# Kernel tuning notes

Hardware: AMD Instinct MI355X
Metric: run time of the kernel (lower is better)

The kernel has to match this reference:

```python
import jax, jax.numpy as jnp
import numpy as np

N_NODES = 50000
N_EDGES = 600000
EMB_DIM = 128
NUM_LAYERS = 5
NUM_ELEM = 118
NUM_CHIR = 4
NUM_BOND_TYPE = 4
NUM_BOND_DIR = 3
BN_EPS = 1e-5


def _xavier(key, shape):
    fan_in, fan_out = shape[0], shape[1]
    limit = np.sqrt(6.0 / (fan_in + fan_out))
    return jax.random.uniform(key, shape, jnp.float32, -limit, limit)


def setup_inputs() -> dict:
    key = jax.random.key(0)
    ks = jax.random.split(key, 12)
    x = jax.random.randint(ks[0], (N_NODES, 2), 0, 4, dtype=jnp.int64)
    edge_index = jax.random.randint(ks[1], (2, N_EDGES), 0, N_NODES, dtype=jnp.int64)
    edge_attr = jax.random.randint(ks[2], (N_EDGES, 2), 0, 3, dtype=jnp.int64)
    elem_emb = _xavier(ks[3], (NUM_ELEM, EMB_DIM))
    chir_emb = _xavier(ks[4], (NUM_CHIR, EMB_DIM))
    bond_type_emb = _xavier(ks[5], (NUM_BOND_TYPE, EMB_DIM))
    bond_dir_emb = _xavier(ks[6], (NUM_BOND_DIR, EMB_DIM))
    # shared GINEConv MLP: Linear(D, 2D) -> ReLU -> Linear(2D, D)
    W1 = _xavier(ks[7], (EMB_DIM, 2 * EMB_DIM))
    b1 = jnp.zeros((2 * EMB_DIM,), jnp.float32)
    W2 = _xavier(ks[8], (2 * EMB_DIM, EMB_DIM))
    b2 = jnp.zeros((EMB_DIM,), jnp.float32)
    # per-layer BatchNorm affine params
    bn_gamma = jnp.ones((NUM_LAYERS, EMB_DIM), jnp.float32)
    bn_beta = jnp.zeros((NUM_LAYERS, EMB_DIM), jnp.float32)
    return {
        "x": x, "edge_index": edge_index, "edge_attr": edge_attr,
        "elem_emb": elem_emb, "chir_emb": chir_emb,
        "bond_type_emb": bond_type_emb, "bond_dir_emb": bond_dir_emb,
        "W1": W1, "b1": b1, "W2": W2, "b2": b2,
        "bn_gamma": bn_gamma, "bn_beta": bn_beta,
    }


def reference(x, edge_index, edge_attr, elem_emb, chir_emb,
              bond_type_emb, bond_dir_emb, W1, b1, W2, b2,
              bn_gamma, bn_beta):
    # input embeddings
    h = elem_emb[x[:, 0]] + chir_emb[x[:, 1]]                    # [N, D]
    e = bond_type_emb[edge_attr[:, 0]] + bond_dir_emb[edge_attr[:, 1]]  # [E, D]
    src, dst = edge_index[0], edge_index[1]
    n = h.shape[0]
    num_layers = bn_gamma.shape[0]
    for layer in range(num_layers):  # conv weights shared across layers
        # GINEConv: msg = relu(x_j + edge_attr), scatter-add, eps=0
        msg = jax.nn.relu(h[src] + e)                            # [E, D]
        agg = jax.ops.segment_sum(msg, dst, num_segments=n)      # [N, D]
        z = h + agg
        out = jax.nn.relu(z @ W1 + b1) @ W2 + b2                 # [N, D]
        # BatchNorm1d (training mode: batch stats, biased variance)
        mean = out.mean(axis=0)
        var = out.var(axis=0)
        out = (out - mean) * jax.lax.rsqrt(var + BN_EPS) * bn_gamma[layer] + bn_beta[layer]
        h = out if layer == num_layers - 1 else jax.nn.relu(out)
    return h
```

## Files before the change

### kernel.cpp

```cpp
#include <hip/hip_runtime.h>

typedef _Float16 f16;
typedef _Float16 f16x8 __attribute__((ext_vector_type(8)));
typedef _Float16 h2 __attribute__((ext_vector_type(2)));
typedef float f32x4 __attribute__((ext_vector_type(4)));
typedef unsigned short u16;
typedef unsigned int u32;

__device__ __forceinline__ float bf2f(u16 b) {
  union { u32 u; float f; } t; t.u = ((u32)b) << 16; return t.f;
}
__device__ __forceinline__ u16 f2bf(float f) {
  union { float f; u32 u; } t; t.f = f;
  u32 u = t.u;
  return (u16)((u + 0x7FFFu + ((u >> 16) & 1u)) >> 16);
}
__device__ __forceinline__ u16 f2h_bits(float f) {
  f16 h = (f16)f;
  union { f16 h; u16 u; } t; t.h = h; return t.u;
}
__device__ __forceinline__ float2 up2(u32 p) {
  union { u32 u; f16 h[2]; } t; t.u = p;
  float2 r; r.x = (float)t.h[0]; r.y = (float)t.h[1]; return r;
}
__device__ __forceinline__ u32 pk2(float x, float y) {
  return (u32)f2h_bits(x) | ((u32)f2h_bits(y) << 16);
}
__device__ __forceinline__ h2 asH2(u32 u) {
  union { u32 u; h2 h; } t; t.u = u; return t.h;
}
__device__ __forceinline__ h2 relu2(h2 a) {
#if __has_builtin(__builtin_elementwise_max)
  h2 z = {(_Float16)0, (_Float16)0};
  return __builtin_elementwise_max(a, z);
#else
  h2 r;
  r.x = a.x > (_Float16)0 ? a.x : (_Float16)0;
  r.y = a.y > (_Float16)0 ? a.y : (_Float16)0;
  return r;
#endif
}

__global__ void k_detect(const u16* __restrict__ elemRaw, const int* __restrict__ eiRaw,
                         int* __restrict__ dflags) {
  __shared__ int bad, nzOdd;
  if (threadIdx.x == 0) { bad = 0; nzOdd = 0; }
  __syncthreads();
  int myBad = 0;
  for (int i = threadIdx.x; i < 4096; i += 256) {
    float v = bf2f(elemRaw[i]);
    if (!(v > -0.2f && v < 0.2f)) myBad++;
  }
  if (myBad) atomicAdd(&bad, myBad);
  int myNz = 0;
  for (int i = threadIdx.x; i < 1024; i += 256)
    if (eiRaw[2 * i + 1] != 0) myNz++;
  if (myNz) atomicAdd(&nzOdd, myNz);
  __syncthreads();
  if (threadIdx.x == 0) {
    dflags[0] = (bad == 0) ? 1 : 0;
    dflags[1] = (nzOdd > 16) ? 1 : 0;
  }
}

__global__ void k_canary(u32* __restrict__ out, const int* __restrict__ dflags,
                         int out_size, u32 pBf, u32 pF32) {
  int isbf = dflags[0];
  int words = isbf ? (out_size >> 1) : out_size;
  int i = blockIdx.x * 256 + threadIdx.x;
  if (i < words) out[i] = isbf ? pBf : pF32;
}

__global__ void k_zero(int* counts, float* stats, int NPad) {
  int i = blockIdx.x * blockDim.x + threadIdx.x;
  if (i < NPad) counts[i] = 0;
  else if (i < NPad + 1280) stats[i - NPad] = 0.f;
}

__global__ void k_cvt(const int* __restrict__ xR, const int* __restrict__ eiR,
                      const int* __restrict__ eaR,
                      const u16* e0, const u16* e1, const u16* e2, const u16* e3,
                      const u16* e4, const u16* e5, const u16* e6, const u16* e7,
                      const u16* e8, const u16* e9,
                      const int* __restrict__ dflags,
                      int* __restrict__ x32, int* __restrict__ ei32, int* __restrict__ combo,
                      int* __restrict__ counts, float* __restrict__ dst,
                      int N, int E, int intBlocks) {
  if ((int)blockIdx.x < intBlocks) {
    int pi = blockIdx.x * 256 + threadIdx.x;
    int nPairs = N + 2 * E;
    if (pi >= nPairs) return;
    int is32 = dflags[1];
    const int* src; int local; int kind;
    if (pi < N) { src = xR; local = pi; kind = 0; }
    else if (pi < N + E) { src = eiR; local = pi - N; kind = 1; }
    else { src = eaR; local = pi - N - E; kind = 2; }
    int j0 = 2 * local;
    int v0, v1;
    if (is32) { int2 v = *(const int2*)(src + j0); v0 = v.x; v1 = v.y; }
    else      { int4 v = *(const int4*)(src + 2 * j0); v0 = v.x; v1 = v.z; }
    if (kind == 0) { x32[j0] = v0; x32[j0 + 1] = v1; }
    else if (kind == 1) {
      ei32[j0] = v0; ei32[j0 + 1] = v1;
      if (j0 >= E) {
        atomicAdd(&counts[v0], 1);
        atomicAdd(&counts[v1], 1);
      }
    } else {
      combo[local] = v0 * 3 + v1;
    }
  } else {
    int i = (blockIdx.x - intBlocks) * 256 + threadIdx.x;
    if (i >= 83712) return;
    int isbf = dflags[0];
    const u16* src; int j;
    if      (i < 15104) { src = e0; j = i; }
    else if (i < 15616) { src = e1; j = i - 15104; }
    else if (i < 16128) { src = e2; j = i - 15616; }
    else if (i < 16512) { src = e3; j = i - 16128; }
    else if (i < 49280) { src = e4; j = i - 16512; }
    else if (i < 49536) { src = e5; j = i - 49280; }
    else if (i < 82304) { src = e6; j = i - 49536; }
    else if (i < 82432) { src = e7; j = i - 82304; }
    else if (i < 83072) { src = e8; j = i - 82432; }
    else                { src = e9; j = i - 83072; }
    dst[i] = isbf ? bf2f(src[j]) : ((const float*)src)[j];
  }
}

__global__ void k_chunksum(const int* __restrict__ counts, int* __restrict__ bsum) {
  int tid = threadIdx.x, lane = tid & 63, w = tid >> 6;
  const int4* c4 = (const int4*)(counts + blockIdx.x * 1024);
  int4 v = c4[tid];
  int s = v.x + v.y + v.z + v.w;
#pragma unroll
  for (int d = 1; d < 64; d <<= 1) s += __shfl_xor(s, d);
  __shared__ int ws[4];
  if (lane == 0) ws[w] = s;
  __syncthreads();
  if (tid == 0) bsum[blockIdx.x] = ws[0] + ws[1] + ws[2] + ws[3];
}

__global__ void k_chunkscan(const int* __restrict__ bsum, int* __restrict__ boff,
                            int* __restrict__ row_start, int N, int nCh) {
  int t = threadIdx.x;
  int v = (t < nCh) ? bsum[t] : 0;
  int incl = v;
#pragma unroll
  for (int d = 1; d < 64; d <<= 1) { int tmp = __shfl_up(incl, d); if (t >= d) incl += tmp; }
  boff[t] = incl - v;
  if (t == 63) row_start[N] = incl;
}

__global__ void k_scanapply(const int* __restrict__ counts, const int* __restrict__ boff,
                            int* __restrict__ row_start, int* __restrict__ cursor, int N) {
  int tid = threadIdx.x, lane = tid & 63, w = tid >> 6;
  int base = blockIdx.x * 1024 + tid * 4;
  int4 v = *(const int4*)(counts + base);
  int tsum = v.x + v.y + v.z + v.w;
  int incl = tsum;
#pragma unroll
  for (int d = 1; d < 64; d <<= 1) { int tmp = __shfl_up(incl, d); if (lane >= d) incl += tmp; }
  __shared__ int ws[4];
  if (lane == 63) ws[w] = incl;
  __syncthreads();
  int woff = 0;
  for (int j = 0; j < w; ++j) woff += ws[j];
  int excl = boff[blockIdx.x] + woff + incl - tsum;
  int e0 = excl, e1 = excl + v.x, e2 = e1 + v.y, e3 = e2 + v.z;
  if (base < N)     { row_start[base] = e0;     cursor[base] = e0; }
  if (base + 1 < N) { row_start[base + 1] = e1; cursor[base + 1] = e1; }
  if (base + 2 < N) { row_start[base + 2] = e2; cursor[base + 2] = e2; }
  if (base + 3 < N) { row_start[base + 3] = e3; cursor[base + 3] = e3; }
}

__global__ void k_scatter(const int* __restrict__ ei, const int* __restrict__ combo,
                          int* cursor, int* packed, int E) {
  int e = blockIdx.x * blockDim.x + threadIdx.x;
  if (e >= E) return;
  int s = ei[e], d = ei[E + e];
  int cb = combo[e];
  int pos = atomicAdd(&cursor[d], 1);
  packed[pos] = s | (cb << 20);
}

__global__ void k_prep(const float* __restrict__ cflt, const int* __restrict__ x,
                       u32* __restrict__ W1F, u32* __restrict__ W2F,
                       u32* __restrict__ tblC, u32* __restrict__ hb, int N, int wtBlocks) {
  if ((int)blockIdx.x < wtBlocks) {
    const float* W1 = cflt + 16512;
    const float* W2 = cflt + 49536;
    const float* bt = cflt + 15616;
    const float* bd = cflt + 16128;
    int g = blockIdx.x * 256 + threadIdx.x;
    {
      int e = g >> 2, wd = g & 3;
      int lane = e & 63, nt = (e >> 6) & 3, ks = (e >> 8) & 3, c = (e >> 10) & 3;
      int q = lane >> 4, lo = lane & 15;
      int n = c * 64 + nt * 16 + lo;
      int k0 = (ks * 4 + q) * 8 + wd * 2;
      W1F[g] = pk2(W1[k0 * 256 + n], W1[(k0 + 1) * 256 + n]);
    }
    {
      int e = g >> 2, wd = g & 3;
      int lane = e & 63, nt = (e >> 6) & 7, ks2 = (e >> 9) & 1, c = (e >> 10) & 3;
      int q = lane >> 4, lo = lane & 15;
      int n2 = nt * 16 + lo;
      int k20 = c * 64 + (ks2 * 4 + q) * 8 + wd * 2;
      W2F[g] = pk2(W2[k20 * 128 + n2], W2[(k20 + 1) * 128 + n2]);
    }
    if (g < 768) {
      int combo = g >> 6, l = g & 63, c0 = l * 2;
      int a0 = combo / 3, a1 = combo - a0 * 3;
      tblC[g] = pk2(bt[a0 * 128 + c0] + bd[a1 * 128 + c0],
                    bt[a0 * 128 + c0 + 1] + bd[a1 * 128 + c0 + 1]);
    }
  } else {
    const float* elem = cflt;
    const float* chir = cflt + 15104;
    int b = blockIdx.x - wtBlocks;
    int wv = (int)(threadIdx.x >> 6);
    int lane = threadIdx.x & 63;
    int node = b * 4 + wv;
    if (node >= N) return;
    int x0 = x[node * 2], x1 = x[node * 2 + 1];
    int c0 = lane * 2;
    float vx = elem[x0 * 128 + c0] + chir[x1 * 128 + c0];
    float vy = elem[x0 * 128 + c0 + 1] + chir[x1 * 128 + c0 + 1];
    hb[(size_t)node * 64 + lane] = pk2(vx, vy);
  }
}

__global__ __launch_bounds__(256) void k_agg(
    const u32* __restrict__ hb, const int* __restrict__ row_start,
    const int* __restrict__ packed, const u32* __restrict__ tblC,
    u32* __restrict__ z, int N) {
  __shared__ u32 tbl[768];
  for (int idx = threadIdx.x; idx < 768; idx += 256) tbl[idx] = tblC[idx];
  __syncthreads();
  const uint4* tbl4 = (const uint4*)tbl;
  const int tid = threadIdx.x;
  const int w = tid >> 6, lane = tid & 63;
  const int sub = lane >> 4, li = lane & 15;
  const int node = blockIdx.x * 16 + w * 4 + sub;
  if (node >= N) return;
  const uint4* hb4 = (const uint4*)hb;
  uint4 sv = hb4[(size_t)node * 16 + li];
  float2 s0 = up2(sv.x), s1 = up2(sv.y), s2 = up2(sv.z), s3 = up2(sv.w);
  float ax0 = s0.x, ay0 = s0.y, ax1 = s1.x, ay1 = s1.y;
  float ax2 = s2.x, ay2 = s2.y, ax3 = s3.x, ay3 = s3.y;
  const int s_ = row_start[node], e_ = row_start[node + 1];
  int p = s_;
  for (; p + 4 <= e_; p += 4) {
    int k0 = packed[p], k1 = packed[p + 1], k2 = packed[p + 2], k3 = packed[p + 3];
    uint4 r0 = hb4[(size_t)(k0 & 0xFFFFF) * 16 + li];
    uint4 r1 = hb4[(size_t)(k1 & 0xFFFFF) * 16 + li];
    uint4 r2 = hb4[(size_t)(k2 & 0xFFFFF) * 16 + li];
    uint4 r3 = hb4[(size_t)(k3 & 0xFFFFF) * 16 + li];
    uint4 t0 = tbl4[(k0 >> 20) * 16 + li];
    uint4 t1 = tbl4[(k1 >> 20) * 16 + li];
    uint4 t2 = tbl4[(k2 >> 20) * 16 + li];
    uint4 t3 = tbl4[(k3 >> 20) * 16 + li];
    h2 m;
    m = relu2(asH2(r0.x) + asH2(t0.x)); ax0 += (float)m.x; ay0 += (float)m.y;
    m = relu2(asH2(r0.y) + asH2(t0.y)); ax1 += (float)m.x; ay1 += (float)m.y;
    m = relu2(asH2(r0.z) + asH2(t0.z)); ax2 += (float)m.x; ay2 += (float)m.y;
    m = relu2(asH2(r0.w) + asH2(t0.w)); ax3 += (float)m.x; ay3 += (float)m.y;
    m = relu2(asH2(r1.x) + asH2(t1.x)); ax0 += (float)m.x; ay0 += (float)m.y;
    m = relu2(asH2(r1.y) + asH2(t1.y)); ax1 += (float)m.x; ay1 += (float)m.y;
    m = relu2(asH2(r1.z) + asH2(t1.z)); ax2 += (float)m.x; ay2 += (float)m.y;
    m = relu2(asH2(r1.w) + asH2(t1.w)); ax3 += (float)m.x; ay3 += (float)m.y;
    m = relu2(asH2(r2.x) + asH2(t2.x)); ax0 += (float)m.x; ay0 += (float)m.y;
    m = relu2(asH2(r2.y) + asH2(t2.y)); ax1 += (float)m.x; ay1 += (float)m.y;
    m = relu2(asH2(r2.z) + asH2(t2.z)); ax2 += (float)m.x; ay2 += (float)m.y;
    m = relu2(asH2(r2.w) + asH2(t2.w)); ax3 += (float)m.x; ay3 += (float)m.y;
    m = relu2(asH2(r3.x) + asH2(t3.x)); ax0 += (float)m.x; ay0 += (float)m.y;
    m = relu2(asH2(r3.y) + asH2(t3.y)); ax1 += (float)m.x; ay1 += (float)m.y;
    m = relu2(asH2(r3.z) + asH2(t3.z)); ax2 += (float)m.x; ay2 += (float)m.y;
    m = relu2(asH2(r3.w) + asH2(t3.w)); ax3 += (float)m.x; ay3 += (float)m.y;
  }
  for (; p < e_; ++p) {
    int k0 = packed[p];
    uint4 r0 = hb4[(size_t)(k0 & 0xFFFFF) * 16 + li];
    uint4 t0 = tbl4[(k0 >> 20) * 16 + li];
    h2 m;
    m = relu2(asH2(r0.x) + asH2(t0.x)); ax0 += (float)m.x; ay0 += (float)m.y;
    m = relu2(asH2(r0.y) + asH2(t0.y)); ax1 += (float)m.x; ay1 += (float)m.y;
    m = relu2(asH2(r0.z) + asH2(t0.z)); ax2 += (float)m.x; ay2 += (float)m.y;
    m = relu2(asH2(r0.w) + asH2(t0.w)); ax3 += (float)m.x; ay3 += (float)m.y;
  }
  uint4 o;
  o.x = pk2(ax0, ay0); o.y = pk2(ax1, ay1); o.z = pk2(ax2, ay2); o.w = pk2(ax3, ay3);
  ((uint4*)z)[(size_t)node * 16 + li] = o;
}

__global__ __launch_bounds__(512, 2) void k_mlp(
    const u16* __restrict__ z, const u32* __restrict__ W1F, const u32* __restrict__ W2F,
    const float* __restrict__ b1, const float* __restrict__ b2,
    u16* __restrict__ act, float* __restrict__ statsL, int N, int nTiles) {
  __shared__ u32 sW1[16384];
  __shared__ u32 sW2[16384];
  __shared__ u16 sYp[8][1024];
  __shared__ float sStats[256];

  const int tid = threadIdx.x;
  const int w = tid >> 6, lane = tid & 63;
  const int lo = lane & 15, q = lane >> 4;

  if (tid < 256) sStats[tid] = 0.f;
  {
    const int4* gW1 = (const int4*)W1F;
    const int4* gW2 = (const int4*)W2F;
    int4* lW1 = (int4*)sW1;
    int4* lW2 = (int4*)sW2;
#pragma unroll
    for (int it = 0; it < 8; ++it) {
      int o = it * 512 + tid;
      lW1[o] = gW1[o];
      lW2[o] = gW2[o];
    }
  }
  __syncthreads();

  float rb1[16], rb2[8];
#pragma unroll
  for (int c = 0; c < 4; ++c)
#pragma unroll
    for (int nt = 0; nt < 4; ++nt)
      rb1[c * 4 + nt] = b1[c * 64 + nt * 16 + lo];
#pragma unroll
  for (int nt = 0; nt < 8; ++nt)
    rb2[nt] = b2[nt * 16 + lo];

  float aSum[8] = {}, aSq[8] = {};
  u16* myY = sYp[w];

  for (int t = blockIdx.x * 8 + w; t < nTiles; t += 2048) {
    const int row0 = t * 16;
    f16x8 a1[4];
    const char* zrow = (const char*)z + (size_t)(row0 + lo) * 256;
#pragma unroll
    for (int ks = 0; ks < 4; ++ks)
      a1[ks] = *(const f16x8*)(zrow + (ks * 4 + q) * 16);

    f32x4 accO[8] = {};
#pragma unroll
    for (int c = 0; c < 4; ++c) {
      f16x8 B1[16];
#pragma unroll
      for (int i = 0; i < 16; ++i)
        B1[i] = *(const f16x8*)((const char*)sW1 + ((c * 16 + i) << 10) + lane * 16);
      f32x4 acc1[4] = {};
#pragma unroll
      for (int ks = 0; ks < 4; ++ks)
#pragma unroll
        for (int nt = 0; nt < 4; ++nt)
          acc1[nt] = __builtin_amdgcn_mfma_f32_16x16x32_f16(a1[ks], B1[ks * 4 + nt], acc1[nt], 0, 0, 0);
#pragma unroll
      for (int nt = 0; nt < 4; ++nt) {
        int ycol = nt * 16 + lo;
        float bias = rb1[c * 4 + nt];
#pragma unroll
        for (int i = 0; i < 4; ++i) {
          int m = q * 4 + i;
          float v = fmaxf(acc1[nt][i] + bias, 0.f);
          myY[m * 64 + (((ycol >> 3) ^ (m & 7)) << 3) + (ycol & 7)] = f2h_bits(v);
        }
      }
      f16x8 B2[16];
#pragma unroll
      for (int i = 0; i < 16; ++i)
        B2[i] = *(const f16x8*)((const char*)sW2 + ((c * 16 + i) << 10) + lane * 16);
#pragma unroll
      for (int ks2 = 0; ks2 < 2; ++ks2) {
        int kq2 = ks2 * 4 + q;
        f16x8 a2 = *(const f16x8*)(myY + lo * 64 + ((kq2 ^ (lo & 7)) << 3));
#pragma unroll
        for (int nt = 0; nt < 8; ++nt)
          accO[nt] = __builtin_amdgcn_mfma_f32_16x16x32_f16(a2, B2[ks2 * 8 + nt], accO[nt], 0, 0, 0);
      }
    }
#pragma unroll
    for (int nt = 0; nt < 8; ++nt) {
      int n2 = nt * 16 + lo;
      float bias = rb2[nt];
#pragma unroll
      for (int i = 0; i < 4; ++i) {
        int row = row0 + q * 4 + i;
        float v = accO[nt][i] + bias;
        act[(size_t)row * 128 + n2] = f2h_bits(v);
        if (row < N) { aSum[nt] += v; aSq[nt] += v * v; }
      }
    }
  }

#pragma unroll
  for (int nt = 0; nt < 8; ++nt) {
    float s = aSum[nt], s2 = aSq[nt];
    s += __shfl_xor(s, 16); s += __shfl_xor(s, 32);
    s2 += __shfl_xor(s2, 16); s2 += __shfl_xor(s2, 32);
    if (q == 0) {
      atomicAdd(&sStats[nt * 16 + lo], s);
      atomicAdd(&sStats[128 + nt * 16 + lo], s2);
    }
  }
  __syncthreads();
  if (tid < 256) atomicAdd(&statsL[tid], sStats[tid]);
}

__global__ __launch_bounds__(256) void k_bnapply(
    const u32* __restrict__ act, const float* __restrict__ statsL,
    const float* __restrict__ gamma, const float* __restrict__ beta,
    float invN, u32* __restrict__ hb, int N) {
  __shared__ float ssc[128], ssh[128];
  int tid = threadIdx.x;
  if (tid < 128) {
    float mean = statsL[tid] * invN;
    float var = statsL[128 + tid] * invN - mean * mean;
    float inv = rsqrtf(var + 1e-5f);
    float scv = gamma[tid] * inv;
    ssc[tid] = scv;
    ssh[tid] = beta[tid] - mean * scv;
  }
  __syncthreads();
  int total = N * 64;
  for (int i = blockIdx.x * 256 + tid; i < total; i += gridDim.x * 256) {
    int c0 = (i & 63) * 2;
    float2 v = up2(act[i]);
    float ox = fmaxf(v.x * ssc[c0] + ssh[c0], 0.f);
    float oy = fmaxf(v.y * ssc[c0 + 1] + ssh[c0 + 1], 0.f);
    hb[i] = pk2(ox, oy);
  }
}

__global__ __launch_bounds__(256) void k_final(
    const u32* __restrict__ act, const float* __restrict__ statsL,
    const float* __restrict__ gamma, const float* __restrict__ beta,
    float invN, const int* __restrict__ dflags, void* __restrict__ outv, int N) {
  __shared__ float ssc[128], ssh[128];
  int tid = threadIdx.x;
  if (tid < 128) {
    float mean = statsL[tid] * invN;
    float var = statsL[128 + tid] * invN - mean * mean;
    float inv = rsqrtf(var + 1e-5f);
    float scv = gamma[tid] * inv;
    ssc[tid] = scv;
    ssh[tid] = beta[tid] - mean * scv;
  }
  __syncthreads();
  int isbf = dflags[0];
  int total = N * 64;
  for (int i = blockIdx.x * 256 + tid; i < total; i += gridDim.x * 256) {
    int c0 = (i & 63) * 2;
    float2 v = up2(act[i]);
    float ox = v.x * ssc[c0] + ssh[c0];
    float oy = v.y * ssc[c0 + 1] + ssh[c0 + 1];
    if (isbf) ((u32*)outv)[i] = (u32)f2bf(ox) | ((u32)f2bf(oy) << 16);
    else { float2 o; o.x = ox; o.y = oy; ((float2*)outv)[i] = o; }
  }
}

extern "C" void kernel_launch(void* const* d_in, const int* in_sizes, int n_in,
                              void* d_out, int out_size, void* d_ws, size_t ws_size,
                              hipStream_t stream) {
  const int* xR  = (const int*)d_in[0];
  const int* eiR = (const int*)d_in[1];
  const int* eaR = (const int*)d_in[2];
  const u16* emR = (const u16*)d_in[3];
  const u16* chR = (const u16*)d_in[4];
  const u16* btR = (const u16*)d_in[5];
  const u16* bdR = (const u16*)d_in[6];
  const u16* W1R = (const u16*)d_in[7];
  const u16* b1R = (const u16*)d_in[8];
  const u16* W2R = (const u16*)d_in[9];
  const u16* b2R = (const u16*)d_in[10];
  const u16* gR  = (const u16*)d_in[11];
  const u16* beR = (const u16*)d_in[12];

  const int N = in_sizes[0] / 2;
  const int E = in_sizes[1] / 2;
  const int L = in_sizes[11] / 128;
  const int Mpad = ((N + 63) / 64) * 64;
  const int nCh = (N + 1023) / 1024;
  const int NPad = nCh * 1024;
  const int nTiles = (N + 15) / 16;

  char* base = (char*)d_ws;
  size_t off = 0;
  auto take = [&](size_t bytes) -> void* {
    void* p = base + off;
    off += (bytes + 255) & ~(size_t)255;
    return p;
  };
  int*   dflags    = (int*)  take(256);
  int*   x32       = (int*)  take((size_t)2 * N * 4);
  int*   ei32      = (int*)  take((size_t)2 * E * 4);
  int*   combo     = (int*)  take((size_t)E * 4);
  float* cflt      = (float*)take(83712 * 4);
  u32*   act       = (u32*)  take((size_t)Mpad * 64 * 4);
  u32*   hb        = (u32*)  take((size_t)Mpad * 64 * 4);
  u16*   zb        = (u16*)  take((size_t)Mpad * 128 * 2);
  int*   packed    = (int*)  take((size_t)E * 4);
  int*   row_start = (int*)  take((size_t)(N + 1) * 4);
  int*   cursor    = (int*)  take((size_t)N * 4);
  int*   counts    = (int*)  take((size_t)NPad * 4);
  int*   bsum      = (int*)  take(64 * 4);
  int*   boff      = (int*)  take(64 * 4);
  float* stats     = (float*)take((size_t)L * 256 * 4);
  u32*   W1F       = (u32*)  take(16384 * 4);
  u32*   W2F       = (u32*)  take(16384 * 4);
  u32*   tblC      = (u32*)  take(768 * 4);
  const size_t need = off;
  (void)n_in;

  float* cB1 = cflt + 49280;
  float* cB2 = cflt + 82304;
  float* cGamma = cflt + 82432;
  float* cBeta = cflt + 83072;

  k_detect<<<dim3(1), dim3(256), 0, stream>>>(emR, eiR, dflags);

  if (need > ws_size) {
    k_canary<<<dim3((out_size + 255) / 256), dim3(256), 0, stream>>>(
        (u32*)d_out, dflags, out_size, 0x40004000u, 0x40000000u);
    return;
  }

  k_zero<<<dim3((NPad + 1280 + 255) / 256), dim3(256), 0, stream>>>(counts, stats, NPad);

  const int nPairs = N + 2 * E;
  const int intBlocks = (nPairs + 255) / 256;
  const int fltBlocks = (83712 + 255) / 256;
  k_cvt<<<dim3(intBlocks + fltBlocks), dim3(256), 0, stream>>>(
      xR, eiR, eaR, emR, chR, btR, bdR, W1R, b1R, W2R, b2R, gR, beR,
      dflags, x32, ei32, combo, counts, cflt, N, E, intBlocks);

  k_chunksum<<<dim3(nCh), dim3(256), 0, stream>>>(counts, bsum);
  k_chunkscan<<<dim3(1), dim3(64), 0, stream>>>(bsum, boff, row_start, N, nCh);
  k_scanapply<<<dim3(nCh), dim3(256), 0, stream>>>(counts, boff, row_start, cursor, N);
  k_scatter<<<dim3((E + 255) / 256), dim3(256), 0, stream>>>(ei32, combo, cursor, packed, E);

  const int wtBlocks = 64;
  k_prep<<<dim3(wtBlocks + (N + 3) / 4), dim3(256), 0, stream>>>(
      cflt, x32, W1F, W2F, tblC, hb, N, wtBlocks);

  const float invN = 1.0f / (float)N;
  for (int l = 0; l < L; ++l) {
    k_agg<<<dim3((N + 15) / 16), dim3(256), 0, stream>>>(
        hb, row_start, packed, tblC, (u32*)zb, N);
    k_mlp<<<dim3(256), dim3(512), 0, stream>>>(
        zb, W1F, W2F, cB1, cB2, (u16*)act, stats + (size_t)l * 256, N, nTiles);
    if (l < L - 1) {
      k_bnapply<<<dim3(1024), dim3(256), 0, stream>>>(
          act, stats + (size_t)l * 256, cGamma + (size_t)l * 128, cBeta + (size_t)l * 128,
          invN, hb, N);
    }
  }
  k_final<<<dim3(1024), dim3(256), 0, stream>>>(
      act, stats + (size_t)(L - 1) * 256, cGamma + (size_t)(L - 1) * 128,
      cBeta + (size_t)(L - 1) * 128, invN, dflags, d_out, N);
}
```

Before: 454.6 us.

## Fuse BatchNorm apply into aggregation gather and merge detect/zero kernels

Drops the separate BN-apply pass. The aggregation kernel now reads the raw MLP output and applies the per-channel scale, shift and ReLU on every gathered neighbour row and on the self row. This removes a full read/write pass over the node features and one launch per layer, at the cost of extra FMA work per edge (about 12 gathers per node). The message math also moves from packed fp16 to fp32, and the detect and zero kernels are merged into one launch.

```diff
diff --git a/kernel.cpp b/kernel.cpp
--- a/kernel.cpp
+++ b/kernel.cpp
@@ -2,7 +2,6 @@
 
 typedef _Float16 f16;
 typedef _Float16 f16x8 __attribute__((ext_vector_type(8)));
-typedef _Float16 h2 __attribute__((ext_vector_type(2)));
 typedef float f32x4 __attribute__((ext_vector_type(4)));
 typedef unsigned short u16;
 typedef unsigned int u32;
@@ -25,20 +24,6 @@
 }
 __device__ __forceinline__ u32 pk2(float x, float y) {
   return (u32)f2h_bits(x) | ((u32)f2h_bits(y) << 16);
-}
-__device__ __forceinline__ h2 asH2(u32 u) {
-  union { u32 u; h2 h; } t; t.u = u; return t.h;
-}
-__device__ __forceinline__ h2 relu2(h2 a) {
-#if __has_builtin(__builtin_elementwise_max)
-  h2 z = {(_Float16)0, (_Float16)0};
-  return __builtin_elementwise_max(a, z);
-#else
-  h2 r;
-  r.x = a.x > (_Float16)0 ? a.x : (_Float16)0;
-  r.y = a.y > (_Float16)0 ? a.y : (_Float16)0;
-  return r;
-#endif
 }
 
 __global__ void k_detect(const u16* __restrict__ elemRaw, const int* __restrict__ eiRaw,
@@ -60,6 +45,35 @@
   if (threadIdx.x == 0) {
     dflags[0] = (bad == 0) ? 1 : 0;
     dflags[1] = (nzOdd > 16) ? 1 : 0;
+  }
+}
+
+__global__ void k_init(const u16* __restrict__ elemRaw, const int* __restrict__ eiRaw,
+                       int* __restrict__ dflags, int* __restrict__ counts,
+                       float* __restrict__ stats, int NPad) {
+  if (blockIdx.x == 0) {
+    __shared__ int bad, nzOdd;
+    if (threadIdx.x == 0) { bad = 0; nzOdd = 0; }
+    __syncthreads();
+    int myBad = 0;
+    for (int i = threadIdx.x; i < 4096; i += 256) {
+      float v = bf2f(elemRaw[i]);
+      if (!(v > -0.2f && v < 0.2f)) myBad++;
+    }
+    if (myBad) atomicAdd(&bad, myBad);
+    int myNz = 0;
+    for (int i = threadIdx.x; i < 1024; i += 256)
+      if (eiRaw[2 * i + 1] != 0) myNz++;
+    if (myNz) atomicAdd(&nzOdd, myNz);
+    __syncthreads();
+    if (threadIdx.x == 0) {
+      dflags[0] = (bad == 0) ? 1 : 0;
+      dflags[1] = (nzOdd > 16) ? 1 : 0;
+    }
+  } else {
+    int i = (blockIdx.x - 1) * 256 + threadIdx.x;
+    if (i < NPad) counts[i] = 0;
+    else if (i < NPad + 1280) stats[i - NPad] = 0.f;
   }
 }
 
@@ -69,12 +83,6 @@
   int words = isbf ? (out_size >> 1) : out_size;
   int i = blockIdx.x * 256 + threadIdx.x;
   if (i < words) out[i] = isbf ? pBf : pF32;
-}
-
-__global__ void k_zero(int* counts, float* stats, int NPad) {
-  int i = blockIdx.x * blockDim.x + threadIdx.x;
-  if (i < NPad) counts[i] = 0;
-  else if (i < NPad + 1280) stats[i - NPad] = 0.f;
 }
 
 __global__ void k_cvt(const int* __restrict__ xR, const int* __restrict__ eiR,
@@ -231,12 +239,27 @@
   }
 }
 
+template <bool BN>
 __global__ __launch_bounds__(256) void k_agg(
-    const u32* __restrict__ hb, const int* __restrict__ row_start,
+    const u32* __restrict__ hsrc, const int* __restrict__ row_start,
     const int* __restrict__ packed, const u32* __restrict__ tblC,
+    const float* __restrict__ statsL, const float* __restrict__ gamma,
+    const float* __restrict__ beta, float invN,
     u32* __restrict__ z, int N) {
   __shared__ u32 tbl[768];
+  __shared__ float ssc[128], ssh[128];
   for (int idx = threadIdx.x; idx < 768; idx += 256) tbl[idx] = tblC[idx];
+  if (BN) {
+    if (threadIdx.x < 128) {
+      int c = threadIdx.x;
+      float mean = statsL[c] * invN;
+      float var = statsL[128 + c] * invN - mean * mean;
+      float inv = rsqrtf(var + 1e-5f);
+      float scv = gamma[c] * inv;
+      ssc[c] = scv;
+      ssh[c] = beta[c] - mean * scv;
+    }
+  }
   __syncthreads();
   const uint4* tbl4 = (const uint4*)tbl;
   const int tid = threadIdx.x;
@@ -244,13 +267,40 @@
   const int sub = lane >> 4, li = lane & 15;
   const int node = blockIdx.x * 16 + w * 4 + sub;
   if (node >= N) return;
-  const uint4* hb4 = (const uint4*)hb;
-  uint4 sv = hb4[(size_t)node * 16 + li];
-  float2 s0 = up2(sv.x), s1 = up2(sv.y), s2 = up2(sv.z), s3 = up2(sv.w);
-  float ax0 = s0.x, ay0 = s0.y, ax1 = s1.x, ay1 = s1.y;
-  float ax2 = s2.x, ay2 = s2.y, ax3 = s3.x, ay3 = s3.y;
+  float sc[8], sh[8];
+  if (BN) {
+#pragma unroll
+    for (int j = 0; j < 8; ++j) { sc[j] = ssc[li * 8 + j]; sh[j] = ssh[li * 8 + j]; }
+  }
+  const uint4* hb4 = (const uint4*)hsrc;
+  float ax0, ay0, ax1, ay1, ax2, ay2, ax3, ay3;
+  {
+    uint4 sv = hb4[(size_t)node * 16 + li];
+    float2 s0 = up2(sv.x), s1 = up2(sv.y), s2 = up2(sv.z), s3 = up2(sv.w);
+    if (BN) {
+      s0.x = fmaxf(fmaf(s0.x, sc[0], sh[0]), 0.f); s0.y = fmaxf(fmaf(s0.y, sc[1], sh[1]), 0.f);
+      s1.x = fmaxf(fmaf(s1.x, sc[2], sh[2]), 0.f); s1.y = fmaxf(fmaf(s1.y, sc[3], sh[3]), 0.f);
+      s2.x = fmaxf(fmaf(s2.x, sc[4], sh[4]), 0.f); s2.y = fmaxf(fmaf(s2.y, sc[5], sh[5]), 0.f);
+      s3.x = fmaxf(fmaf(s3.x, sc[6], sh[6]), 0.f); s3.y = fmaxf(fmaf(s3.y, sc[7], sh[7]), 0.f);
+    }
+    ax0 = s0.x; ay0 = s0.y; ax1 = s1.x; ay1 = s1.y;
+    ax2 = s2.x; ay2 = s2.y; ax3 = s3.x; ay3 = s3.y;
+  }
   const int s_ = row_start[node], e_ = row_start[node + 1];
   int p = s_;
+
+#define ACCP(RW, TW, I0, AX, AY)                                       \
+  {                                                                    \
+    float2 rv = up2(RW); float2 tv = up2(TW);                          \
+    float hx, hy;                                                      \
+    if (BN) {                                                          \
+      hx = fmaxf(fmaf(rv.x, sc[I0], sh[I0]), 0.f);                     \
+      hy = fmaxf(fmaf(rv.y, sc[I0 + 1], sh[I0 + 1]), 0.f);             \
+    } else { hx = rv.x; hy = rv.y; }                                   \
+    AX += fmaxf(hx + tv.x, 0.f);                                       \
+    AY += fmaxf(hy + tv.y, 0.f);                                       \
+  }
+
   for (; p + 4 <= e_; p += 4) {
     int k0 = packed[p], k1 = packed[p + 1], k2 = packed[p + 2], k3 = packed[p + 3];
     uint4 r0 = hb4[(size_t)(k0 & 0xFFFFF) * 16 + li];
@@ -261,34 +311,33 @@
     uint4 t1 = tbl4[(k1 >> 20) * 16 + li];
     uint4 t2 = tbl4[(k2 >> 20) * 16 + li];
     uint4 t3 = tbl4[(k3 >> 20) * 16 + li];
-    h2 m;
-    m = relu2(asH2(r0.x) + asH2(t0.x)); ax0 += (float)m.x; ay0 += (float)m.y;
-    m = relu2(asH2(r0.y) + asH2(t0.y)); ax1 += (float)m.x; ay1 += (float)m.y;
-    m = relu2(asH2(r0.z) + asH2(t0.z)); ax2 += (float)m.x; ay2 += (float)m.y;
-    m = relu2(asH2(r0.w) + asH2(t0.w)); ax3 += (float)m.x; ay3 += (float)m.y;
-    m = relu2(asH2(r1.x) + asH2(t1.x)); ax0 += (float)m.x; ay0 += (float)m.y;
-    m = relu2(asH2(r1.y) + asH2(t1.y)); ax1 += (float)m.x; ay1 += (float)m.y;
-    m = relu2(asH2(r1.z) + asH2(t1.z)); ax2 += (float)m.x; ay2 += (float)m.y;
-    m = relu2(asH2(r1.w) + asH2(t1.w)); ax3 += (float)m.x; ay3 += (float)m.y;
-    m = relu2(asH2(r2.x) + asH2(t2.x)); ax0 += (float)m.x; ay0 += (float)m.y;
-    m = relu2(asH2(r2.y) + asH2(t2.y)); ax1 += (float)m.x; ay1 += (float)m.y;
-    m = relu2(asH2(r2.z) + asH2(t2.z)); ax2 += (float)m.x; ay2 += (float)m.y;
-    m = relu2(asH2(r2.w) + asH2(t2.w)); ax3 += (float)m.x; ay3 += (float)m.y;
-    m = relu2(asH2(r3.x) + asH2(t3.x)); ax0 += (float)m.x; ay0 += (float)m.y;
-    m = relu2(asH2(r3.y) + asH2(t3.y)); ax1 += (float)m.x; ay1 += (float)m.y;
-    m = relu2(asH2(r3.z) + asH2(t3.z)); ax2 += (float)m.x; ay2 += (float)m.y;
-    m = relu2(asH2(r3.w) + asH2(t3.w)); ax3 += (float)m.x; ay3 += (float)m.y;
+    ACCP(r0.x, t0.x, 0, ax0, ay0)
+    ACCP(r0.y, t0.y, 2, ax1, ay1)
+    ACCP(r0.z, t0.z, 4, ax2, ay2)
+    ACCP(r0.w, t0.w, 6, ax3, ay3)
+    ACCP(r1.x, t1.x, 0, ax0, ay0)
+    ACCP(r1.y, t1.y, 2, ax1, ay1)
+    ACCP(r1.z, t1.z, 4, ax2, ay2)
+    ACCP(r1.w, t1.w, 6, ax3, ay3)
+    ACCP(r2.x, t2.x, 0, ax0, ay0)
+    ACCP(r2.y, t2.y, 2, ax1, ay1)
+    ACCP(r2.z, t2.z, 4, ax2, ay2)
+    ACCP(r2.w, t2.w, 6, ax3, ay3)
+    ACCP(r3.x, t3.x, 0, ax0, ay0)
+    ACCP(r3.y, t3.y, 2, ax1, ay1)
+    ACCP(r3.z, t3.z, 4, ax2, ay2)
+    ACCP(r3.w, t3.w, 6, ax3, ay3)
   }
   for (; p < e_; ++p) {
     int k0 = packed[p];
     uint4 r0 = hb4[(size_t)(k0 & 0xFFFFF) * 16 + li];
     uint4 t0 = tbl4[(k0 >> 20) * 16 + li];
-    h2 m;
-    m = relu2(asH2(r0.x) + asH2(t0.x)); ax0 += (float)m.x; ay0 += (float)m.y;
-    m = relu2(asH2(r0.y) + asH2(t0.y)); ax1 += (float)m.x; ay1 += (float)m.y;
-    m = relu2(asH2(r0.z) + asH2(t0.z)); ax2 += (float)m.x; ay2 += (float)m.y;
-    m = relu2(asH2(r0.w) + asH2(t0.w)); ax3 += (float)m.x; ay3 += (float)m.y;
-  }
+    ACCP(r0.x, t0.x, 0, ax0, ay0)
+    ACCP(r0.y, t0.y, 2, ax1, ay1)
+    ACCP(r0.z, t0.z, 4, ax2, ay2)
+    ACCP(r0.w, t0.w, 6, ax3, ay3)
+  }
+#undef ACCP
   uint4 o;
   o.x = pk2(ax0, ay0); o.y = pk2(ax1, ay1); o.z = pk2(ax2, ay2); o.w = pk2(ax3, ay3);
   ((uint4*)z)[(size_t)node * 16 + li] = o;
@@ -406,31 +455,6 @@
   }
   __syncthreads();
   if (tid < 256) atomicAdd(&statsL[tid], sStats[tid]);
-}
-
-__global__ __launch_bounds__(256) void k_bnapply(
-    const u32* __restrict__ act, const float* __restrict__ statsL,
-    const float* __restrict__ gamma, const float* __restrict__ beta,
-    float invN, u32* __restrict__ hb, int N) {
-  __shared__ float ssc[128], ssh[128];
-  int tid = threadIdx.x;
-  if (tid < 128) {
-    float mean = statsL[tid] * invN;
-    float var = statsL[128 + tid] * invN - mean * mean;
-    float inv = rsqrtf(var + 1e-5f);
-    float scv = gamma[tid] * inv;
-    ssc[tid] = scv;
-    ssh[tid] = beta[tid] - mean * scv;
-  }
-  __syncthreads();
-  int total = N * 64;
-  for (int i = blockIdx.x * 256 + tid; i < total; i += gridDim.x * 256) {
-    int c0 = (i & 63) * 2;
-    float2 v = up2(act[i]);
-    float ox = fmaxf(v.x * ssc[c0] + ssh[c0], 0.f);
-    float oy = fmaxf(v.y * ssc[c0 + 1] + ssh[c0 + 1], 0.f);
-    hb[i] = pk2(ox, oy);
-  }
 }
 
 __global__ __launch_bounds__(256) void k_final(
@@ -518,15 +542,15 @@
   float* cGamma = cflt + 82432;
   float* cBeta = cflt + 83072;
 
-  k_detect<<<dim3(1), dim3(256), 0, stream>>>(emR, eiR, dflags);
-
   if (need > ws_size) {
+    k_detect<<<dim3(1), dim3(256), 0, stream>>>(emR, eiR, dflags);
     k_canary<<<dim3((out_size + 255) / 256), dim3(256), 0, stream>>>(
         (u32*)d_out, dflags, out_size, 0x40004000u, 0x40000000u);
     return;
   }
 
-  k_zero<<<dim3((NPad + 1280 + 255) / 256), dim3(256), 0, stream>>>(counts, stats, NPad);
+  const int nzBlocks = (NPad + 1280 + 255) / 256;
+  k_init<<<dim3(nzBlocks + 1), dim3(256), 0, stream>>>(emR, eiR, dflags, counts, stats, NPad);
 
   const int nPairs = N + 2 * E;
   const int intBlocks = (nPairs + 255) / 256;
@@ -546,15 +570,17 @@
 
   const float invN = 1.0f / (float)N;
   for (int l = 0; l < L; ++l) {
-    k_agg<<<dim3((N + 15) / 16), dim3(256), 0, stream>>>(
-        hb, row_start, packed, tblC, (u32*)zb, N);
+    if (l == 0) {
+      k_agg<false><<<dim3((N + 15) / 16), dim3(256), 0, stream>>>(
+          hb, row_start, packed, tblC, nullptr, nullptr, nullptr, 0.f, (u32*)zb, N);
+    } else {
+      k_agg<true><<<dim3((N + 15) / 16), dim3(256), 0, stream>>>(
+          act, row_start, packed, tblC, stats + (size_t)(l - 1) * 256,
+          cGamma + (size_t)(l - 1) * 128, cBeta + (size_t)(l - 1) * 128, invN,
+          (u32*)zb, N);
+    }
     k_mlp<<<dim3(256), dim3(512), 0, stream>>>(
         zb, W1F, W2F, cB1, cB2, (u16*)act, stats + (size_t)l * 256, N, nTiles);
-    if (l < L - 1) {
-      k_bnapply<<<dim3(1024), dim3(256), 0, stream>>>(
-          act, stats + (size_t)l * 256, cGamma + (size_t)l * 128, cBeta + (size_t)l * 128,
-          invN, hb, N);
-    }
   }
   k_final<<<dim3(1024), dim3(256), 0, stream>>>(
       act, stats + (size_t)(L - 1) * 256, cGamma + (size_t)(L - 1) * 128,
```

After: 460.1 us. No clear change (+1.2%).

## Replace global BN stat atomics with per-block partials and merge init kernels

Applied to the files above, without the earlier changes.

k_mlp now writes its per-block BatchNorm sums into a partial buffer instead of doing global float atomics. k_bnapply and k_final reduce the 256 partials per block themselves, and their grids shrink from 1024 to 256 blocks to limit that redundant reduction work. The detect and zero kernels are fused into one init launch, which removes a launch and the need to zero the stats buffer. This avoids atomic contention and gives a deterministic reduction, at the cost of every apply block reading 256KB of partials.

```diff
diff --git a/kernel.cpp b/kernel.cpp
--- a/kernel.cpp
+++ b/kernel.cpp
@@ -63,18 +63,39 @@
   }
 }
 
+__global__ void k_init(const u16* __restrict__ elemRaw, const int* __restrict__ eiRaw,
+                       int* __restrict__ dflags, int* __restrict__ counts, int NPad) {
+  if (blockIdx.x == 0) {
+    __shared__ int bad, nzOdd;
+    if (threadIdx.x == 0) { bad = 0; nzOdd = 0; }
+    __syncthreads();
+    int myBad = 0;
+    for (int i = threadIdx.x; i < 4096; i += 256) {
+      float v = bf2f(elemRaw[i]);
+      if (!(v > -0.2f && v < 0.2f)) myBad++;
+    }
+    if (myBad) atomicAdd(&bad, myBad);
+    int myNz = 0;
+    for (int i = threadIdx.x; i < 1024; i += 256)
+      if (eiRaw[2 * i + 1] != 0) myNz++;
+    if (myNz) atomicAdd(&nzOdd, myNz);
+    __syncthreads();
+    if (threadIdx.x == 0) {
+      dflags[0] = (bad == 0) ? 1 : 0;
+      dflags[1] = (nzOdd > 16) ? 1 : 0;
+    }
+  } else {
+    int i = (blockIdx.x - 1) * 256 + threadIdx.x;
+    if (i < NPad) counts[i] = 0;
+  }
+}
+
 __global__ void k_canary(u32* __restrict__ out, const int* __restrict__ dflags,
                          int out_size, u32 pBf, u32 pF32) {
   int isbf = dflags[0];
   int words = isbf ? (out_size >> 1) : out_size;
   int i = blockIdx.x * 256 + threadIdx.x;
   if (i < words) out[i] = isbf ? pBf : pF32;
-}
-
-__global__ void k_zero(int* counts, float* stats, int NPad) {
-  int i = blockIdx.x * blockDim.x + threadIdx.x;
-  if (i < NPad) counts[i] = 0;
-  else if (i < NPad + 1280) stats[i - NPad] = 0.f;
 }
 
 __global__ void k_cvt(const int* __restrict__ xR, const int* __restrict__ eiR,
@@ -297,7 +318,7 @@
 __global__ __launch_bounds__(512, 2) void k_mlp(
     const u16* __restrict__ z, const u32* __restrict__ W1F, const u32* __restrict__ W2F,
     const float* __restrict__ b1, const float* __restrict__ b2,
-    u16* __restrict__ act, float* __restrict__ statsL, int N, int nTiles) {
+    u16* __restrict__ act, float* __restrict__ statsP, int N, int nTiles) {
   __shared__ u32 sW1[16384];
   __shared__ u32 sW2[16384];
   __shared__ u16 sYp[8][1024];
@@ -405,18 +426,26 @@
     }
   }
   __syncthreads();
-  if (tid < 256) atomicAdd(&statsL[tid], sStats[tid]);
+  if (tid < 256) statsP[blockIdx.x * 256 + tid] = sStats[tid];
 }
 
 __global__ __launch_bounds__(256) void k_bnapply(
-    const u32* __restrict__ act, const float* __restrict__ statsL,
+    const u32* __restrict__ act, const float* __restrict__ statsP,
     const float* __restrict__ gamma, const float* __restrict__ beta,
     float invN, u32* __restrict__ hb, int N) {
+  __shared__ float sTot[256];
   __shared__ float ssc[128], ssh[128];
   int tid = threadIdx.x;
+  {
+    float acc = 0.f;
+#pragma unroll 8
+    for (int b = 0; b < 256; ++b) acc += statsP[b * 256 + tid];
+    sTot[tid] = acc;
+  }
+  __syncthreads();
   if (tid < 128) {
-    float mean = statsL[tid] * invN;
-    float var = statsL[128 + tid] * invN - mean * mean;
+    float mean = sTot[tid] * invN;
+    float var = sTot[128 + tid] * invN - mean * mean;
     float inv = rsqrtf(var + 1e-5f);
     float scv = gamma[tid] * inv;
     ssc[tid] = scv;
@@ -434,14 +463,22 @@
 }
 
 __global__ __launch_bounds__(256) void k_final(
-    const u32* __restrict__ act, const float* __restrict__ statsL,
+    const u32* __restrict__ act, const float* __restrict__ statsP,
     const float* __restrict__ gamma, const float* __restrict__ beta,
     float invN, const int* __restrict__ dflags, void* __restrict__ outv, int N) {
+  __shared__ float sTot[256];
   __shared__ float ssc[128], ssh[128];
   int tid = threadIdx.x;
+  {
+    float acc = 0.f;
+#pragma unroll 8
+    for (int b = 0; b < 256; ++b) acc += statsP[b * 256 + tid];
+    sTot[tid] = acc;
+  }
+  __syncthreads();
   if (tid < 128) {
-    float mean = statsL[tid] * invN;
-    float var = statsL[128 + tid] * invN - mean * mean;
+    float mean = sTot[tid] * invN;
+    float var = sTot[128 + tid] * invN - mean * mean;
     float inv = rsqrtf(var + 1e-5f);
     float scv = gamma[tid] * inv;
     ssc[tid] = scv;
@@ -506,7 +543,7 @@
   int*   counts    = (int*)  take((size_t)NPad * 4);
   int*   bsum      = (int*)  take(64 * 4);
   int*   boff      = (int*)  take(64 * 4);
-  float* stats     = (float*)take((size_t)L * 256 * 4);
+  float* statsP    = (float*)take((size_t)256 * 256 * 4);
   u32*   W1F       = (u32*)  take(16384 * 4);
   u32*   W2F       = (u32*)  take(16384 * 4);
   u32*   tblC      = (u32*)  take(768 * 4);
@@ -518,15 +555,15 @@
   float* cGamma = cflt + 82432;
   float* cBeta = cflt + 83072;
 
-  k_detect<<<dim3(1), dim3(256), 0, stream>>>(emR, eiR, dflags);
-
   if (need > ws_size) {
+    k_detect<<<dim3(1), dim3(256), 0, stream>>>(emR, eiR, dflags);
     k_canary<<<dim3((out_size + 255) / 256), dim3(256), 0, stream>>>(
         (u32*)d_out, dflags, out_size, 0x40004000u, 0x40000000u);
     return;
   }
 
-  k_zero<<<dim3((NPad + 1280 + 255) / 256), dim3(256), 0, stream>>>(counts, stats, NPad);
+  const int nzBlocks = (NPad + 255) / 256;
+  k_init<<<dim3(nzBlocks + 1), dim3(256), 0, stream>>>(emR, eiR, dflags, counts, NPad);
 
   const int nPairs = N + 2 * E;
   const int intBlocks = (nPairs + 255) / 256;
@@ -549,14 +586,14 @@
     k_agg<<<dim3((N + 15) / 16), dim3(256), 0, stream>>>(
         hb, row_start, packed, tblC, (u32*)zb, N);
     k_mlp<<<dim3(256), dim3(512), 0, stream>>>(
-        zb, W1F, W2F, cB1, cB2, (u16*)act, stats + (size_t)l * 256, N, nTiles);
+        zb, W1F, W2F, cB1, cB2, (u16*)act, statsP, N, nTiles);
     if (l < L - 1) {
-      k_bnapply<<<dim3(1024), dim3(256), 0, stream>>>(
-          act, stats + (size_t)l * 256, cGamma + (size_t)l * 128, cBeta + (size_t)l * 128,
+      k_bnapply<<<dim3(256), dim3(256), 0, stream>>>(
+          act, statsP, cGamma + (size_t)l * 128, cBeta + (size_t)l * 128,
           invN, hb, N);
     }
   }
-  k_final<<<dim3(1024), dim3(256), 0, stream>>>(
-      act, stats + (size_t)(L - 1) * 256, cGamma + (size_t)(L - 1) * 128,
+  k_final<<<dim3(256), dim3(256), 0, stream>>>(
+      act, statsP, cGamma + (size_t)(L - 1) * 128,
       cBeta + (size_t)(L - 1) * 128, invN, dflags, d_out, N);
 }
```

After: 550.1 us. +21.0%, slower.
